# Kernel optimization log

Measured on AMD Instinct MI355X. Metric: run time of the kernel, lower is better.

## Reference

```python
import jax, jax.numpy as jnp
import numpy as np

N_USER = 50000
N_POST = 50000
E = 400000
IN_DIM = 128
HID = 64
HEADS = 4
OUT_DIM = 64
NEG_SLOPE = 0.2


def _xavier(key, shape):
    fan_in, fan_out = shape[0], shape[-1]
    lim = float(np.sqrt(6.0 / (fan_in + fan_out)))
    return jax.random.uniform(key, shape, jnp.float32, -lim, lim)


def setup_inputs() -> dict:
    key = jax.random.key(0)
    ks = jax.random.split(key, 24)
    inp = {}
    inp['x_user'] = jax.random.normal(ks[0], (N_USER, IN_DIM), jnp.float32)
    inp['x_post'] = jax.random.normal(ks[1], (N_POST, IN_DIM), jnp.float32)
    inp['src_u2u'] = jax.random.randint(ks[2], (E,), 0, N_USER, jnp.int32)
    inp['dst_u2u'] = jax.random.randint(ks[3], (E,), 0, N_USER, jnp.int32)
    inp['src_p2u'] = jax.random.randint(ks[4], (E,), 0, N_POST, jnp.int32)
    inp['dst_p2u'] = jax.random.randint(ks[5], (E,), 0, N_USER, jnp.int32)
    inp['src_u2p'] = jax.random.randint(ks[6], (E,), 0, N_USER, jnp.int32)
    inp['dst_u2p'] = jax.random.randint(ks[7], (E,), 0, N_POST, jnp.int32)
    # shared input projection (nn.Linear(in_dim, hidden_dim), xavier W, zero b)
    inp['W_proj'] = _xavier(ks[8], (IN_DIM, HID))
    inp['b_proj'] = jnp.zeros((HID,), jnp.float32)
    # per-edge-type GATConv params: lin [HID, HEADS*HID], att vectors [HEADS, HID], bias [HEADS*HID]
    for i, et in enumerate(['u2u', 'p2u', 'u2p']):
        inp['lin_' + et] = _xavier(ks[9 + 3 * i], (HID, HEADS * HID))
        inp['att_src_' + et] = _xavier(ks[10 + 3 * i], (HEADS, HID))
        inp['att_dst_' + et] = _xavier(ks[11 + 3 * i], (HEADS, HID))
        inp['bias_' + et] = jnp.zeros((HEADS * HID,), jnp.float32)
    inp['W_out'] = _xavier(ks[20], (HEADS * HID, OUT_DIM))
    inp['b_out'] = jnp.zeros((OUT_DIM,), jnp.float32)
    return inp


def _gat_conv(h_src_nodes, h_dst_nodes, src, dst, lin, att_src, att_dst, bias, n_dst):
    # h_*_nodes: [N, HID] projected node features
    hs = (h_src_nodes @ lin).reshape(-1, HEADS, HID)   # [Ns, H, C]
    hd = (h_dst_nodes @ lin).reshape(-1, HEADS, HID)   # [Nd, H, C]
    a_s = jnp.sum(hs * att_src, axis=-1)               # [Ns, H]
    a_d = jnp.sum(hd * att_dst, axis=-1)               # [Nd, H]
    e = jax.nn.leaky_relu(a_s[src] + a_d[dst], NEG_SLOPE)  # [E, H]
    # per-destination segment softmax
    m = jax.lax.stop_gradient(jax.ops.segment_max(e, dst, num_segments=n_dst))
    ex = jnp.exp(e - m[dst])
    s = jax.ops.segment_sum(ex, dst, num_segments=n_dst)
    alpha = ex / (s[dst] + 1e-16)                      # [E, H]
    msg = hs[src] * alpha[:, :, None]                  # [E, H, C]
    out = jax.ops.segment_sum(msg, dst, num_segments=n_dst)  # [Nd, H, C]
    return out.reshape(n_dst, HEADS * HID) + bias


def reference(x_user, x_post, src_u2u, dst_u2u, src_p2u, dst_p2u, src_u2p, dst_u2p,
              W_proj, b_proj,
              lin_u2u, att_src_u2u, att_dst_u2u, bias_u2u,
              lin_p2u, att_src_p2u, att_dst_p2u, bias_p2u,
              lin_u2p, att_src_u2p, att_dst_u2p, bias_u2p,
              W_out, b_out):
    hu = x_user @ W_proj + b_proj   # [N_USER, HID]
    hp = x_post @ W_proj + b_proj   # [N_POST, HID]
    # HeteroConv(aggr='sum'): sum conv outputs sharing the same dst type
    out_user = (_gat_conv(hu, hu, src_u2u, dst_u2u, lin_u2u, att_src_u2u, att_dst_u2u, bias_u2u, N_USER)
                + _gat_conv(hp, hu, src_p2u, dst_p2u, lin_p2u, att_src_p2u, att_dst_p2u, bias_p2u, N_USER))
    out_post = _gat_conv(hu, hp, src_u2p, dst_u2p, lin_u2p, att_src_u2p, att_dst_u2p, bias_u2p, N_POST)
    out_user = jax.nn.elu(out_user)
    out_post = jax.nn.elu(out_post)
    out_user = out_user @ W_out + b_out   # [N_USER, OUT_DIM]
    return (out_user, out_post)
```

## Files before the change

### kernel.cpp

```cpp
#include <hip/hip_runtime.h>
#include <math.h>

#define IN_DIM 128
#define HID 64
#define HEADS 4
#define HH 256
#define OUT_DIM 64
#define NEG_SLOPE 0.2f

typedef unsigned short ushort_t;
using bf16x8 = __attribute__((ext_vector_type(8))) short;
using f32x4  = __attribute__((ext_vector_type(4))) float;

__device__ __forceinline__ float elu_f(float x){ return x > 0.f ? x : (expf(x) - 1.f); }
__device__ __forceinline__ float lrelu_f(float x){ return fmaxf(x, NEG_SLOPE * x); }

__device__ __forceinline__ ushort_t f2bf(float x){
  unsigned u = __float_as_uint(x);
  unsigned r = (u + 0x7fffu + ((u >> 16) & 1u)) >> 16;
  return (ushort_t)r;
}
__device__ __forceinline__ float bf2f(ushort_t v){ return __uint_as_float(((unsigned)v) << 16); }

__global__ void proj_kernel(const float* __restrict__ xu, const float* __restrict__ xp,
                            const float* __restrict__ W, const float* __restrict__ b,
                            float* __restrict__ hu, float* __restrict__ hp,
                            int n_user, int n_total){
  __shared__ float xs[16 * IN_DIM];
  int row0 = blockIdx.x * 16;
  for (int i = threadIdx.x; i < 16 * IN_DIM; i += 256){
    int r = row0 + i / IN_DIM;
    float v = 0.f;
    if (r < n_total){
      int k = i % IN_DIM;
      v = (r < n_user) ? xu[(size_t)r * IN_DIM + k] : xp[(size_t)(r - n_user) * IN_DIM + k];
    }
    xs[i] = v;
  }
  __syncthreads();
  int c = threadIdx.x & 63;
  int g = threadIdx.x >> 6;
  float acc[4] = {0.f, 0.f, 0.f, 0.f};
  for (int k = 0; k < IN_DIM; ++k){
    float wv = W[k * HID + c];
    #pragma unroll
    for (int r = 0; r < 4; ++r) acc[r] += xs[(g * 4 + r) * IN_DIM + k] * wv;
  }
  float bb = b[c];
  #pragma unroll
  for (int r = 0; r < 4; ++r){
    int rr = row0 + g * 4 + r;
    if (rr < n_total){
      float v = acc[r] + bb;
      if (rr < n_user) hu[(size_t)rr * HID + c] = v;
      else             hp[(size_t)(rr - n_user) * HID + c] = v;
    }
  }
}

__global__ void fold3_kernel(const float* __restrict__ lin0, const float* __restrict__ as0, const float* __restrict__ ad0,
                             const float* __restrict__ lin1, const float* __restrict__ as1, const float* __restrict__ ad1,
                             const float* __restrict__ lin2, const float* __restrict__ as2, const float* __restrict__ ad2,
                             float* __restrict__ wbuf){
  int t = blockIdx.x;
  const float* lin = t == 0 ? lin0 : (t == 1 ? lin1 : lin2);
  const float* as  = t == 0 ? as0  : (t == 1 ? as1  : as2);
  const float* ad  = t == 0 ? ad0  : (t == 1 ? ad1  : ad2);
  int tid = threadIdx.x;
  int h = tid >> 6, k = tid & 63;
  float vs = 0.f, vd = 0.f;
  for (int c = 0; c < HID; ++c){
    float lv = lin[k * HH + h * HID + c];
    vs += lv * as[h * HID + c];
    vd += lv * ad[h * HID + c];
  }
  wbuf[(t * 2 + 0) * HH + tid] = vs;
  wbuf[(t * 2 + 1) * HH + tid] = vd;
}

__global__ void att6_kernel(const float* __restrict__ hu, const float* __restrict__ hp,
                            const float* __restrict__ wbuf, float* __restrict__ abuf,
                            int n_user, int n_post, int n_max){
  long gw = ((long)blockIdx.x * blockDim.x + threadIdx.x) >> 6;
  int lane = threadIdx.x & 63;
  int seg, node;
  long r = gw;
  int nu = n_user, np_ = n_post;
  if      (r < nu)            { seg = 0; node = (int)r; }
  else if ((r -= nu) < nu)    { seg = 1; node = (int)r; }
  else if ((r -= nu) < np_)   { seg = 2; node = (int)r; }
  else if ((r -= np_) < nu)   { seg = 3; node = (int)r; }
  else if ((r -= nu) < nu)    { seg = 4; node = (int)r; }
  else if ((r -= nu) < np_)   { seg = 5; node = (int)r; }
  else return;
  const float* h = (seg == 2 || seg == 5) ? hp : hu;
  const float* w = wbuf + seg * HH;
  float* outp = abuf + (size_t)seg * n_max * HEADS;
  float hv = h[(size_t)node * HID + lane];
  #pragma unroll
  for (int hh = 0; hh < HEADS; ++hh){
    float p = hv * w[hh * HID + lane];
    #pragma unroll
    for (int off = 32; off > 0; off >>= 1) p += __shfl_xor(p, off, 64);
    if (lane == 0) outp[(size_t)node * HEADS + hh] = p;
  }
}

__global__ void hist3_kernel(const int* __restrict__ d0, const int* __restrict__ d1,
                             const int* __restrict__ d2, int* __restrict__ deg3,
                             int E0, int E1, int E2, int b1_, int b2_){
  int e = blockIdx.x * blockDim.x + threadIdx.x;
  int ET = E0 + E1 + E2;
  if (e >= ET) return;
  int idx;
  if (e < E0)            idx = d0[e];
  else if (e < E0 + E1)  idx = b1_ + d1[e - E0];
  else                   idx = b2_ + d2[e - E0 - E1];
  atomicAdd(deg3 + idx, 1);
}

__global__ void scan1_kernel(const int* __restrict__ deg, int* __restrict__ offs,
                             int* __restrict__ bsum, int n){
  __shared__ int sm[256];
  int i = blockIdx.x * 256 + threadIdx.x;
  int v = (i < n) ? deg[i] : 0;
  sm[threadIdx.x] = v;
  __syncthreads();
  for (int off = 1; off < 256; off <<= 1){
    int t = (threadIdx.x >= off) ? sm[threadIdx.x - off] : 0;
    __syncthreads();
    sm[threadIdx.x] += t;
    __syncthreads();
  }
  if (i < n) offs[i] = sm[threadIdx.x] - v;
  if (threadIdx.x == 255) bsum[blockIdx.x] = sm[255];
}

__global__ void scan2_kernel(int* __restrict__ bsum, int nb){
  __shared__ int sm[1024];
  int v = (threadIdx.x < nb) ? bsum[threadIdx.x] : 0;
  sm[threadIdx.x] = v;
  __syncthreads();
  for (int off = 1; off < 1024; off <<= 1){
    int t = (threadIdx.x >= off) ? sm[threadIdx.x - off] : 0;
    __syncthreads();
    sm[threadIdx.x] += t;
    __syncthreads();
  }
  if (threadIdx.x < nb) bsum[threadIdx.x] = sm[threadIdx.x] - v;
}

__global__ void scan3_kernel(int* __restrict__ offs, int* __restrict__ cursor,
                             const int* __restrict__ bsum, int n){
  int i = blockIdx.x * 256 + threadIdx.x;
  if (i >= n) return;
  int o = offs[i] + bsum[blockIdx.x];
  offs[i] = o;
  cursor[i] = o;
}

__global__ void csrfill3_kernel(const int* __restrict__ s0, const int* __restrict__ d0,
                                const int* __restrict__ s1, const int* __restrict__ d1,
                                const int* __restrict__ s2, const int* __restrict__ d2,
                                int* __restrict__ cursor, int* __restrict__ csr_src,
                                int E0, int E1, int E2, int b1_, int b2_){
  int e = blockIdx.x * blockDim.x + threadIdx.x;
  int ET = E0 + E1 + E2;
  if (e >= ET) return;
  int sidx, didx;
  if (e < E0){ sidx = s0[e]; didx = d0[e]; }
  else if (e < E0 + E1){ int ee = e - E0; sidx = s1[ee]; didx = b1_ + d1[ee]; }
  else { int ee = e - E0 - E1; sidx = s2[ee]; didx = b2_ + d2[ee]; }
  int pos = atomicAdd(cursor + didx, 1);
  csr_src[pos] = sidx;
}

__global__ void gather_all_kernel(const int* __restrict__ csr_src, const int* __restrict__ offs3,
                                  const int* __restrict__ deg3,
                                  const float* __restrict__ hu, const float* __restrict__ hp,
                                  const float* __restrict__ abuf,
                                  int n_user, int n_post, int n_max,
                                  ushort_t* __restrict__ aggA, ushort_t* __restrict__ aggB,
                                  ushort_t* __restrict__ aggC){
  int gw = blockIdx.x * 4 + (threadIdx.x >> 6);
  int lane = threadIdx.x & 63;
  int n3 = 2 * n_user + n_post;
  if (gw >= n3) return;
  const float* h_src; const float4* as4; const float4* ad4; ushort_t* agg; int dloc;
  size_t astr = (size_t)n_max * HEADS;
  if (gw < n_user){
    dloc = gw; h_src = hu;
    as4 = (const float4*)(abuf + 0 * astr); ad4 = (const float4*)(abuf + 1 * astr); agg = aggA;
  } else if (gw < 2 * n_user){
    dloc = gw - n_user; h_src = hp;
    as4 = (const float4*)(abuf + 2 * astr); ad4 = (const float4*)(abuf + 3 * astr); agg = aggB;
  } else {
    dloc = gw - 2 * n_user; h_src = hu;
    as4 = (const float4*)(abuf + 4 * astr); ad4 = (const float4*)(abuf + 5 * astr); agg = aggC;
  }
  int base = offs3[gw], n = deg3[gw];
  float4 adv = ad4[dloc];
  float s0 = 0.f, s1 = 0.f, s2 = 0.f, s3 = 0.f;
  float a0 = 0.f, a1 = 0.f, a2 = 0.f, a3 = 0.f;
  float hA = 0.f, hB = 0.f;
  float4 aA = make_float4(0,0,0,0), aB = make_float4(0,0,0,0);
  if (n > 0){ int s = csr_src[base];     hA = h_src[(size_t)s * HID + lane]; aA = as4[s]; }
  if (n > 1){ int s = csr_src[base + 1]; hB = h_src[(size_t)s * HID + lane]; aB = as4[s]; }
  for (int j = 0; j < n; ++j){
    float hv = hA; float4 av = aA;
    hA = hB; aA = aB;
    if (j + 2 < n){
      int s = csr_src[base + j + 2];
      hB = h_src[(size_t)s * HID + lane]; aB = as4[s];
    }
    float p0 = __expf(lrelu_f(av.x + adv.x));
    float p1 = __expf(lrelu_f(av.y + adv.y));
    float p2 = __expf(lrelu_f(av.z + adv.z));
    float p3 = __expf(lrelu_f(av.w + adv.w));
    s0 += p0; s1 += p1; s2 += p2; s3 += p3;
    a0 = fmaf(p0, hv, a0); a1 = fmaf(p1, hv, a1);
    a2 = fmaf(p2, hv, a2); a3 = fmaf(p3, hv, a3);
  }
  a0 *= 1.f / (s0 + 1e-16f); a1 *= 1.f / (s1 + 1e-16f);
  a2 *= 1.f / (s2 + 1e-16f); a3 *= 1.f / (s3 + 1e-16f);
  size_t o = (size_t)dloc * HH + lane;
  agg[o + 0 * HID] = f2bf(a0);
  agg[o + 1 * HID] = f2bf(a1);
  agg[o + 2 * HID] = f2bf(a2);
  agg[o + 3 * HID] = f2bf(a3);
}

__global__ void prep_kernel(const float* __restrict__ L0, const float* __restrict__ L1,
                            const float* __restrict__ L2, const float* __restrict__ Wo,
                            const float* __restrict__ b0, const float* __restrict__ b1,
                            ushort_t* __restrict__ Wt0, ushort_t* __restrict__ Wt1,
                            ushort_t* __restrict__ Wt2, ushort_t* __restrict__ Wot,
                            float* __restrict__ bsum){
  int g = blockIdx.x * 256 + threadIdx.x;
  if (g < 49152){
    int m = g >> 14;
    int i = g & 16383;
    int h = i >> 12, rem = i & 4095;
    int o = rem >> 6, c = rem & 63;
    const float* L = m == 0 ? L0 : (m == 1 ? L1 : L2);
    ushort_t* W = m == 0 ? Wt0 : (m == 1 ? Wt1 : Wt2);
    W[i] = f2bf(L[(size_t)c * HH + h * 64 + o]);
  } else if (g < 65536){
    int i = g - 49152;
    int o = i >> 8, k = i & 255;
    Wot[i] = f2bf(Wo[(size_t)k * OUT_DIM + o]);
  } else if (g < 65792){
    int i = g - 65536;
    bsum[i] = b0[i] + b1[i];
  }
}

__global__ void user_epi_mfma(const ushort_t* __restrict__ aggA, const ushort_t* __restrict__ aggB,
                              const ushort_t* __restrict__ Wt0, const ushort_t* __restrict__ Wt1,
                              const ushort_t* __restrict__ Wot, const float* __restrict__ bsum,
                              const float* __restrict__ bo, float* __restrict__ out, int n){
  __shared__ ushort_t Tl[64 * 256];
  int tid = threadIdx.x;
  int w = tid >> 6, lane = tid & 63;
  int l15 = lane & 15, kg = lane >> 4;
  int row0 = blockIdx.x * 64 + w * 16;

  int ar = row0 + l15; if (ar > n - 1) ar = n - 1;
  #pragma unroll
  for (int h = 0; h < HEADS; ++h){
    const ushort_t* pa = aggA + (size_t)ar * HH + h * 64 + kg * 8;
    const ushort_t* pb = aggB + (size_t)ar * HH + h * 64 + kg * 8;
    bf16x8 aA0 = *(const bf16x8*)pa;
    bf16x8 aA1 = *(const bf16x8*)(pa + 32);
    bf16x8 aB0 = *(const bf16x8*)pb;
    bf16x8 aB1 = *(const bf16x8*)(pb + 32);
    #pragma unroll
    for (int n16 = 0; n16 < 4; ++n16){
      int o = n16 * 16 + l15;
      const ushort_t* w0 = Wt0 + h * 4096 + o * 64 + kg * 8;
      const ushort_t* w1 = Wt1 + h * 4096 + o * 64 + kg * 8;
      f32x4 acc = {0.f, 0.f, 0.f, 0.f};
      acc = __builtin_amdgcn_mfma_f32_16x16x32_bf16(aA0, *(const bf16x8*)w0, acc, 0, 0, 0);
      acc = __builtin_amdgcn_mfma_f32_16x16x32_bf16(aA1, *(const bf16x8*)(w0 + 32), acc, 0, 0, 0);
      acc = __builtin_amdgcn_mfma_f32_16x16x32_bf16(aB0, *(const bf16x8*)w1, acc, 0, 0, 0);
      acc = __builtin_amdgcn_mfma_f32_16x16x32_bf16(aB1, *(const bf16x8*)(w1 + 32), acc, 0, 0, 0);
      int col = h * 64 + n16 * 16 + l15;
      float bb = bsum[col];
      #pragma unroll
      for (int j = 0; j < 4; ++j){
        int rl = w * 16 + kg * 4 + j;
        float v = elu_f(acc[j] + bb);
        int byteoff = rl * 512 + ((col * 2) ^ ((rl & 7) << 4));
        Tl[byteoff >> 1] = f2bf(v);
      }
    }
  }
  __syncthreads();

  int rl = w * 16 + l15;
  #pragma unroll
  for (int nf = 0; nf < 4; ++nf){
    f32x4 acc = {0.f, 0.f, 0.f, 0.f};
    const ushort_t* wp = Wot + (nf * 16 + l15) * 256 + kg * 8;
    #pragma unroll
    for (int ks = 0; ks < 8; ++ks){
      int ab = rl * 512 + ((ks * 64 + kg * 16) ^ ((rl & 7) << 4));
      bf16x8 a = *(const bf16x8*)((const char*)Tl + ab);
      acc = __builtin_amdgcn_mfma_f32_16x16x32_bf16(a, *(const bf16x8*)(wp + ks * 32), acc, 0, 0, 0);
    }
    int colo = nf * 16 + l15;
    float bb = bo[colo];
    #pragma unroll
    for (int j = 0; j < 4; ++j){
      int row = blockIdx.x * 64 + w * 16 + kg * 4 + j;
      if (row < n) out[(size_t)row * OUT_DIM + colo] = acc[j] + bb;
    }
  }
}

__global__ void post_epi_mfma(const ushort_t* __restrict__ aggC, const ushort_t* __restrict__ Wt2,
                              const float* __restrict__ b2, float* __restrict__ out, int n){
  int tid = threadIdx.x;
  int w = tid >> 6, lane = tid & 63;
  int l15 = lane & 15, kg = lane >> 4;
  int row0 = blockIdx.x * 64 + w * 16;
  int ar = row0 + l15; if (ar > n - 1) ar = n - 1;
  #pragma unroll
  for (int h = 0; h < HEADS; ++h){
    const ushort_t* pa = aggC + (size_t)ar * HH + h * 64 + kg * 8;
    bf16x8 a0 = *(const bf16x8*)pa;
    bf16x8 a1 = *(const bf16x8*)(pa + 32);
    #pragma unroll
    for (int n16 = 0; n16 < 4; ++n16){
      int o = n16 * 16 + l15;
      const ushort_t* w2 = Wt2 + h * 4096 + o * 64 + kg * 8;
      f32x4 acc = {0.f, 0.f, 0.f, 0.f};
      acc = __builtin_amdgcn_mfma_f32_16x16x32_bf16(a0, *(const bf16x8*)w2, acc, 0, 0, 0);
      acc = __builtin_amdgcn_mfma_f32_16x16x32_bf16(a1, *(const bf16x8*)(w2 + 32), acc, 0, 0, 0);
      int col = h * 64 + n16 * 16 + l15;
      float bb = b2[col];
      #pragma unroll
      for (int j = 0; j < 4; ++j){
        int row = row0 + kg * 4 + j;
        if (row < n) out[(size_t)row * HH + col] = elu_f(acc[j] + bb);
      }
    }
  }
}

extern "C" void kernel_launch(void* const* d_in, const int* in_sizes, int n_in,
                              void* d_out, int out_size, void* d_ws, size_t ws_size,
                              hipStream_t stream){
  const float* xu = (const float*)d_in[0];
  const float* xp = (const float*)d_in[1];
  const float* Wp = (const float*)d_in[8];
  const float* bp = (const float*)d_in[9];
  const float* Wo = (const float*)d_in[22];
  const float* bo = (const float*)d_in[23];

  const int n_user = in_sizes[0] / IN_DIM;
  const int n_post = in_sizes[1] / IN_DIM;
  const int n_max  = n_user > n_post ? n_user : n_post;
  const int E0 = in_sizes[2], E1 = in_sizes[4], E2 = in_sizes[6];
  const int ET = E0 + E1 + E2;
  const int n3 = n_user + n_user + n_post;
  float* out = (float*)d_out;

  float* ws = (float*)d_ws;
  size_t off = 0;
  float* hu       = ws + off; off += (size_t)n_user * HID;
  float* hp       = ws + off; off += (size_t)n_post * HID;
  float* abuf     = ws + off; off += (size_t)6 * n_max * HEADS;
  float* wbuf     = ws + off; off += 6 * HH;
  ushort_t* aggA  = (ushort_t*)(ws + off); off += ((size_t)n_max * HH + 1) / 2;
  ushort_t* aggB  = (ushort_t*)(ws + off); off += ((size_t)n_max * HH + 1) / 2;
  ushort_t* aggC  = (ushort_t*)(ws + off); off += ((size_t)n_max * HH + 1) / 2;
  ushort_t* Wt0   = (ushort_t*)(ws + off); off += 8192;
  ushort_t* Wt1   = (ushort_t*)(ws + off); off += 8192;
  ushort_t* Wt2   = (ushort_t*)(ws + off); off += 8192;
  ushort_t* Wot   = (ushort_t*)(ws + off); off += 8192;
  float* bsum_u   = ws + off; off += 256;
  int* deg3       = (int*)(ws + off); off += n3;
  int* offs3      = (int*)(ws + off); off += n3;
  int* cursor3    = (int*)(ws + off); off += n3;
  int* bsum       = (int*)(ws + off); off += 1024;
  int* csr_src    = (int*)(ws + off); off += ET;

  int n_total = n_user + n_post;
  proj_kernel<<<(n_total + 15) / 16, 256, 0, stream>>>(xu, xp, Wp, bp, hu, hp, n_user, n_total);

  prep_kernel<<<258, 256, 0, stream>>>(
      (const float*)d_in[10], (const float*)d_in[14], (const float*)d_in[18], Wo,
      (const float*)d_in[13], (const float*)d_in[17], Wt0, Wt1, Wt2, Wot, bsum_u);

  fold3_kernel<<<3, 256, 0, stream>>>(
      (const float*)d_in[10], (const float*)d_in[11], (const float*)d_in[12],
      (const float*)d_in[14], (const float*)d_in[15], (const float*)d_in[16],
      (const float*)d_in[18], (const float*)d_in[19], (const float*)d_in[20], wbuf);

  long waves6 = 4L * n_user + 2L * n_post;
  att6_kernel<<<(int)((waves6 + 3) / 4), 256, 0, stream>>>(hu, hp, wbuf, abuf, n_user, n_post, n_max);

  hipMemsetAsync(deg3, 0, (size_t)n3 * sizeof(int), stream);
  hist3_kernel<<<(ET + 255) / 256, 256, 0, stream>>>(
      (const int*)d_in[3], (const int*)d_in[5], (const int*)d_in[7],
      deg3, E0, E1, E2, n_user, 2 * n_user);
  int nb = (n3 + 255) / 256;
  scan1_kernel<<<nb, 256, 0, stream>>>(deg3, offs3, bsum, n3);
  scan2_kernel<<<1, 1024, 0, stream>>>(bsum, nb);
  scan3_kernel<<<nb, 256, 0, stream>>>(offs3, cursor3, bsum, n3);
  csrfill3_kernel<<<(ET + 255) / 256, 256, 0, stream>>>(
      (const int*)d_in[2], (const int*)d_in[3],
      (const int*)d_in[4], (const int*)d_in[5],
      (const int*)d_in[6], (const int*)d_in[7],
      cursor3, csr_src, E0, E1, E2, n_user, 2 * n_user);

  gather_all_kernel<<<(n3 + 3) / 4, 256, 0, stream>>>(
      csr_src, offs3, deg3, hu, hp, abuf, n_user, n_post, n_max, aggA, aggB, aggC);

  user_epi_mfma<<<(n_user + 63) / 64, 256, 0, stream>>>(
      aggA, aggB, Wt0, Wt1, Wot, bsum_u, bo, out, n_user);

  post_epi_mfma<<<(n_post + 63) / 64, 256, 0, stream>>>(
      aggC, Wt2, (const float*)d_in[21], out + (size_t)n_user * OUT_DIM, n_post);
}
```

Before: 632.7 us.

## Use MFMA bf16 input projection, bf16 node features, and precomputed per-edge alpha

Replaces the scalar FP32 input projection with a bf16 MFMA kernel whose weights are transposed in prep. The projected node features are now stored as bf16, which halves the gather traffic. The softmax is split out: a thread-per-node kernel computes normalized per-edge attention weights into a new float4 alpha buffer, and the gather kernel then only does weighted sums. This adds a kernel launch and an extra read and write of 1.2M float4 alphas, and lowers feature precision to bf16.

```diff
diff --git a/kernel.cpp b/kernel.cpp
--- a/kernel.cpp
+++ b/kernel.cpp
@@ -22,38 +22,89 @@
 }
 __device__ __forceinline__ float bf2f(ushort_t v){ return __uint_as_float(((unsigned)v) << 16); }
 
-__global__ void proj_kernel(const float* __restrict__ xu, const float* __restrict__ xp,
-                            const float* __restrict__ W, const float* __restrict__ b,
-                            float* __restrict__ hu, float* __restrict__ hp,
-                            int n_user, int n_total){
-  __shared__ float xs[16 * IN_DIM];
-  int row0 = blockIdx.x * 16;
-  for (int i = threadIdx.x; i < 16 * IN_DIM; i += 256){
-    int r = row0 + i / IN_DIM;
-    float v = 0.f;
-    if (r < n_total){
-      int k = i % IN_DIM;
-      v = (r < n_user) ? xu[(size_t)r * IN_DIM + k] : xp[(size_t)(r - n_user) * IN_DIM + k];
-    }
-    xs[i] = v;
+__global__ void prep_kernel(const float* __restrict__ L0, const float* __restrict__ L1,
+                            const float* __restrict__ L2, const float* __restrict__ Wo,
+                            const float* __restrict__ Wp,
+                            const float* __restrict__ b0, const float* __restrict__ b1,
+                            ushort_t* __restrict__ Wt0, ushort_t* __restrict__ Wt1,
+                            ushort_t* __restrict__ Wt2, ushort_t* __restrict__ Wot,
+                            ushort_t* __restrict__ Wpt, float* __restrict__ bsum){
+  int g = blockIdx.x * 256 + threadIdx.x;
+  if (g < 49152){
+    int m = g >> 14;
+    int i = g & 16383;
+    int h = i >> 12, rem = i & 4095;
+    int o = rem >> 6, c = rem & 63;
+    const float* L = m == 0 ? L0 : (m == 1 ? L1 : L2);
+    ushort_t* W = m == 0 ? Wt0 : (m == 1 ? Wt1 : Wt2);
+    W[i] = f2bf(L[(size_t)c * HH + h * 64 + o]);
+  } else if (g < 65536){
+    int i = g - 49152;
+    int o = i >> 8, k = i & 255;
+    Wot[i] = f2bf(Wo[(size_t)k * OUT_DIM + o]);
+  } else if (g < 73728){
+    int i = g - 65536;
+    int c = i >> 7, k = i & 127;
+    Wpt[i] = f2bf(Wp[(size_t)k * HID + c]);
+  } else if (g < 73984){
+    int i = g - 73728;
+    bsum[i] = b0[i] + b1[i];
+  }
+}
+
+__global__ void proj_mfma(const float* __restrict__ xu, const float* __restrict__ xp,
+                          const ushort_t* __restrict__ Wpt, const float* __restrict__ b,
+                          ushort_t* __restrict__ hu, ushort_t* __restrict__ hp,
+                          int n_user, int n_total){
+  __shared__ ushort_t xs[64 * 128];
+  int tid = threadIdx.x;
+  int row0 = blockIdx.x * 64;
+  #pragma unroll
+  for (int p = 0; p < 4; ++p){
+    int idx = (p * 256 + tid) * 8;
+    int r = idx >> 7, k = idx & 127;
+    int gr = row0 + r;
+    float4 v0 = make_float4(0,0,0,0), v1 = make_float4(0,0,0,0);
+    if (gr < n_total){
+      const float* src = (gr < n_user) ? (xu + (size_t)gr * IN_DIM + k)
+                                       : (xp + (size_t)(gr - n_user) * IN_DIM + k);
+      v0 = *(const float4*)src; v1 = *(const float4*)(src + 4);
+    }
+    bf16x8 bv;
+    bv[0] = (short)f2bf(v0.x); bv[1] = (short)f2bf(v0.y);
+    bv[2] = (short)f2bf(v0.z); bv[3] = (short)f2bf(v0.w);
+    bv[4] = (short)f2bf(v1.x); bv[5] = (short)f2bf(v1.y);
+    bv[6] = (short)f2bf(v1.z); bv[7] = (short)f2bf(v1.w);
+    int byteoff = r * 256 + ((k * 2) ^ ((r & 7) << 4));
+    *(bf16x8*)((char*)xs + byteoff) = bv;
   }
   __syncthreads();
-  int c = threadIdx.x & 63;
-  int g = threadIdx.x >> 6;
-  float acc[4] = {0.f, 0.f, 0.f, 0.f};
-  for (int k = 0; k < IN_DIM; ++k){
-    float wv = W[k * HID + c];
-    #pragma unroll
-    for (int r = 0; r < 4; ++r) acc[r] += xs[(g * 4 + r) * IN_DIM + k] * wv;
-  }
-  float bb = b[c];
-  #pragma unroll
-  for (int r = 0; r < 4; ++r){
-    int rr = row0 + g * 4 + r;
-    if (rr < n_total){
-      float v = acc[r] + bb;
-      if (rr < n_user) hu[(size_t)rr * HID + c] = v;
-      else             hp[(size_t)(rr - n_user) * HID + c] = v;
+  int w = tid >> 6, lane = tid & 63, l15 = lane & 15, kg = lane >> 4;
+  int arow = w * 16 + l15;
+  bf16x8 afrag[4];
+  #pragma unroll
+  for (int ks = 0; ks < 4; ++ks){
+    int k = ks * 32 + kg * 8;
+    int byteoff = arow * 256 + ((k * 2) ^ ((arow & 7) << 4));
+    afrag[ks] = *(const bf16x8*)((const char*)xs + byteoff);
+  }
+  #pragma unroll
+  for (int n16 = 0; n16 < 4; ++n16){
+    f32x4 acc = {0.f, 0.f, 0.f, 0.f};
+    const ushort_t* wp = Wpt + (n16 * 16 + l15) * 128;
+    #pragma unroll
+    for (int ks = 0; ks < 4; ++ks)
+      acc = __builtin_amdgcn_mfma_f32_16x16x32_bf16(afrag[ks], *(const bf16x8*)(wp + ks * 32 + kg * 8), acc, 0, 0, 0);
+    int col = n16 * 16 + l15;
+    float bb = b[col];
+    #pragma unroll
+    for (int j = 0; j < 4; ++j){
+      int row = row0 + w * 16 + kg * 4 + j;
+      if (row < n_total){
+        ushort_t hv = f2bf(acc[j] + bb);
+        if (row < n_user) hu[(size_t)row * HID + col] = hv;
+        else              hp[(size_t)(row - n_user) * HID + col] = hv;
+      }
     }
   }
 }
@@ -78,7 +129,7 @@
   wbuf[(t * 2 + 1) * HH + tid] = vd;
 }
 
-__global__ void att6_kernel(const float* __restrict__ hu, const float* __restrict__ hp,
+__global__ void att6_kernel(const ushort_t* __restrict__ hu, const ushort_t* __restrict__ hp,
                             const float* __restrict__ wbuf, float* __restrict__ abuf,
                             int n_user, int n_post, int n_max){
   long gw = ((long)blockIdx.x * blockDim.x + threadIdx.x) >> 6;
@@ -93,10 +144,10 @@
   else if ((r -= nu) < nu)    { seg = 4; node = (int)r; }
   else if ((r -= nu) < np_)   { seg = 5; node = (int)r; }
   else return;
-  const float* h = (seg == 2 || seg == 5) ? hp : hu;
+  const ushort_t* h = (seg == 2 || seg == 5) ? hp : hu;
   const float* w = wbuf + seg * HH;
   float* outp = abuf + (size_t)seg * n_max * HEADS;
-  float hv = h[(size_t)node * HID + lane];
+  float hv = bf2f(h[(size_t)node * HID + lane]);
   #pragma unroll
   for (int hh = 0; hh < HEADS; ++hh){
     float p = hv * w[hh * HID + lane];
@@ -175,84 +226,72 @@
   csr_src[pos] = sidx;
 }
 
-__global__ void gather_all_kernel(const int* __restrict__ csr_src, const int* __restrict__ offs3,
-                                  const int* __restrict__ deg3,
-                                  const float* __restrict__ hu, const float* __restrict__ hp,
-                                  const float* __restrict__ abuf,
-                                  int n_user, int n_post, int n_max,
-                                  ushort_t* __restrict__ aggA, ushort_t* __restrict__ aggB,
-                                  ushort_t* __restrict__ aggC){
+__global__ void stats_alpha_kernel(const int* __restrict__ csr_src, const int* __restrict__ offs3,
+                                   const int* __restrict__ deg3, const float* __restrict__ abuf,
+                                   float4* __restrict__ alpha,
+                                   int n_user, int n_post, int n_max){
+  int gw = blockIdx.x * 256 + threadIdx.x;
+  int n3 = 2 * n_user + n_post;
+  if (gw >= n3) return;
+  size_t astr = (size_t)n_max;
+  const float4* as4; const float4* ad4; int dloc;
+  const float4* ab = (const float4*)abuf;
+  if (gw < n_user){ dloc = gw; as4 = ab; ad4 = ab + astr; }
+  else if (gw < 2 * n_user){ dloc = gw - n_user; as4 = ab + 2 * astr; ad4 = ab + 3 * astr; }
+  else { dloc = gw - 2 * n_user; as4 = ab + 4 * astr; ad4 = ab + 5 * astr; }
+  int base = offs3[gw], n = deg3[gw];
+  float4 ad = ad4[dloc];
+  float s0 = 0.f, s1 = 0.f, s2 = 0.f, s3 = 0.f;
+  for (int j = 0; j < n; ++j){
+    float4 a = as4[csr_src[base + j]];
+    s0 += __expf(lrelu_f(a.x + ad.x));
+    s1 += __expf(lrelu_f(a.y + ad.y));
+    s2 += __expf(lrelu_f(a.z + ad.z));
+    s3 += __expf(lrelu_f(a.w + ad.w));
+  }
+  float i0 = 1.f / (s0 + 1e-16f), i1 = 1.f / (s1 + 1e-16f);
+  float i2 = 1.f / (s2 + 1e-16f), i3 = 1.f / (s3 + 1e-16f);
+  for (int j = 0; j < n; ++j){
+    float4 a = as4[csr_src[base + j]];
+    alpha[base + j] = make_float4(__expf(lrelu_f(a.x + ad.x)) * i0,
+                                  __expf(lrelu_f(a.y + ad.y)) * i1,
+                                  __expf(lrelu_f(a.z + ad.z)) * i2,
+                                  __expf(lrelu_f(a.w + ad.w)) * i3);
+  }
+}
+
+__global__ void gather_slim(const int* __restrict__ csr_src, const int* __restrict__ offs3,
+                            const int* __restrict__ deg3,
+                            const ushort_t* __restrict__ hu, const ushort_t* __restrict__ hp,
+                            const float4* __restrict__ alpha,
+                            int n_user, int n_post,
+                            ushort_t* __restrict__ aggA, ushort_t* __restrict__ aggB,
+                            ushort_t* __restrict__ aggC){
   int gw = blockIdx.x * 4 + (threadIdx.x >> 6);
   int lane = threadIdx.x & 63;
   int n3 = 2 * n_user + n_post;
   if (gw >= n3) return;
-  const float* h_src; const float4* as4; const float4* ad4; ushort_t* agg; int dloc;
-  size_t astr = (size_t)n_max * HEADS;
-  if (gw < n_user){
-    dloc = gw; h_src = hu;
-    as4 = (const float4*)(abuf + 0 * astr); ad4 = (const float4*)(abuf + 1 * astr); agg = aggA;
-  } else if (gw < 2 * n_user){
-    dloc = gw - n_user; h_src = hp;
-    as4 = (const float4*)(abuf + 2 * astr); ad4 = (const float4*)(abuf + 3 * astr); agg = aggB;
-  } else {
-    dloc = gw - 2 * n_user; h_src = hu;
-    as4 = (const float4*)(abuf + 4 * astr); ad4 = (const float4*)(abuf + 5 * astr); agg = aggC;
-  }
+  const ushort_t* h; ushort_t* agg; int dloc;
+  if (gw < n_user){ dloc = gw; h = hu; agg = aggA; }
+  else if (gw < 2 * n_user){ dloc = gw - n_user; h = hp; agg = aggB; }
+  else { dloc = gw - 2 * n_user; h = hu; agg = aggC; }
   int base = offs3[gw], n = deg3[gw];
-  float4 adv = ad4[dloc];
-  float s0 = 0.f, s1 = 0.f, s2 = 0.f, s3 = 0.f;
   float a0 = 0.f, a1 = 0.f, a2 = 0.f, a3 = 0.f;
   float hA = 0.f, hB = 0.f;
-  float4 aA = make_float4(0,0,0,0), aB = make_float4(0,0,0,0);
-  if (n > 0){ int s = csr_src[base];     hA = h_src[(size_t)s * HID + lane]; aA = as4[s]; }
-  if (n > 1){ int s = csr_src[base + 1]; hB = h_src[(size_t)s * HID + lane]; aB = as4[s]; }
+  if (n > 0) hA = bf2f(h[(size_t)csr_src[base] * HID + lane]);
+  if (n > 1) hB = bf2f(h[(size_t)csr_src[base + 1] * HID + lane]);
   for (int j = 0; j < n; ++j){
-    float hv = hA; float4 av = aA;
-    hA = hB; aA = aB;
-    if (j + 2 < n){
-      int s = csr_src[base + j + 2];
-      hB = h_src[(size_t)s * HID + lane]; aB = as4[s];
-    }
-    float p0 = __expf(lrelu_f(av.x + adv.x));
-    float p1 = __expf(lrelu_f(av.y + adv.y));
-    float p2 = __expf(lrelu_f(av.z + adv.z));
-    float p3 = __expf(lrelu_f(av.w + adv.w));
-    s0 += p0; s1 += p1; s2 += p2; s3 += p3;
-    a0 = fmaf(p0, hv, a0); a1 = fmaf(p1, hv, a1);
-    a2 = fmaf(p2, hv, a2); a3 = fmaf(p3, hv, a3);
-  }
-  a0 *= 1.f / (s0 + 1e-16f); a1 *= 1.f / (s1 + 1e-16f);
-  a2 *= 1.f / (s2 + 1e-16f); a3 *= 1.f / (s3 + 1e-16f);
+    float hv = hA; hA = hB;
+    if (j + 2 < n) hB = bf2f(h[(size_t)csr_src[base + j + 2] * HID + lane]);
+    float4 al = alpha[base + j];
+    a0 = fmaf(al.x, hv, a0); a1 = fmaf(al.y, hv, a1);
+    a2 = fmaf(al.z, hv, a2); a3 = fmaf(al.w, hv, a3);
+  }
   size_t o = (size_t)dloc * HH + lane;
   agg[o + 0 * HID] = f2bf(a0);
   agg[o + 1 * HID] = f2bf(a1);
   agg[o + 2 * HID] = f2bf(a2);
   agg[o + 3 * HID] = f2bf(a3);
-}
-
-__global__ void prep_kernel(const float* __restrict__ L0, const float* __restrict__ L1,
-                            const float* __restrict__ L2, const float* __restrict__ Wo,
-                            const float* __restrict__ b0, const float* __restrict__ b1,
-                            ushort_t* __restrict__ Wt0, ushort_t* __restrict__ Wt1,
-                            ushort_t* __restrict__ Wt2, ushort_t* __restrict__ Wot,
-                            float* __restrict__ bsum){
-  int g = blockIdx.x * 256 + threadIdx.x;
-  if (g < 49152){
-    int m = g >> 14;
-    int i = g & 16383;
-    int h = i >> 12, rem = i & 4095;
-    int o = rem >> 6, c = rem & 63;
-    const float* L = m == 0 ? L0 : (m == 1 ? L1 : L2);
-    ushort_t* W = m == 0 ? Wt0 : (m == 1 ? Wt1 : Wt2);
-    W[i] = f2bf(L[(size_t)c * HH + h * 64 + o]);
-  } else if (g < 65536){
-    int i = g - 49152;
-    int o = i >> 8, k = i & 255;
-    Wot[i] = f2bf(Wo[(size_t)k * OUT_DIM + o]);
-  } else if (g < 65792){
-    int i = g - 65536;
-    bsum[i] = b0[i] + b1[i];
-  }
 }
 
 __global__ void user_epi_mfma(const ushort_t* __restrict__ aggA, const ushort_t* __restrict__ aggB,
@@ -368,30 +407,34 @@
 
   float* ws = (float*)d_ws;
   size_t off = 0;
-  float* hu       = ws + off; off += (size_t)n_user * HID;
-  float* hp       = ws + off; off += (size_t)n_post * HID;
+  ushort_t* hu    = (ushort_t*)(ws + off); off += (size_t)n_user * HID / 2;
+  ushort_t* hp    = (ushort_t*)(ws + off); off += (size_t)n_post * HID / 2;
   float* abuf     = ws + off; off += (size_t)6 * n_max * HEADS;
   float* wbuf     = ws + off; off += 6 * HH;
-  ushort_t* aggA  = (ushort_t*)(ws + off); off += ((size_t)n_max * HH + 1) / 2;
-  ushort_t* aggB  = (ushort_t*)(ws + off); off += ((size_t)n_max * HH + 1) / 2;
-  ushort_t* aggC  = (ushort_t*)(ws + off); off += ((size_t)n_max * HH + 1) / 2;
+  ushort_t* aggA  = (ushort_t*)(ws + off); off += (size_t)n_max * HH / 2;
+  ushort_t* aggB  = (ushort_t*)(ws + off); off += (size_t)n_max * HH / 2;
+  ushort_t* aggC  = (ushort_t*)(ws + off); off += (size_t)n_max * HH / 2;
   ushort_t* Wt0   = (ushort_t*)(ws + off); off += 8192;
   ushort_t* Wt1   = (ushort_t*)(ws + off); off += 8192;
   ushort_t* Wt2   = (ushort_t*)(ws + off); off += 8192;
   ushort_t* Wot   = (ushort_t*)(ws + off); off += 8192;
+  ushort_t* Wpt   = (ushort_t*)(ws + off); off += 4096;
   float* bsum_u   = ws + off; off += 256;
   int* deg3       = (int*)(ws + off); off += n3;
   int* offs3      = (int*)(ws + off); off += n3;
   int* cursor3    = (int*)(ws + off); off += n3;
   int* bsum       = (int*)(ws + off); off += 1024;
   int* csr_src    = (int*)(ws + off); off += ET;
+  off = (off + 3) & ~(size_t)3;
+  float4* alpha   = (float4*)(ws + off); off += (size_t)ET * 4;
 
   int n_total = n_user + n_post;
-  proj_kernel<<<(n_total + 15) / 16, 256, 0, stream>>>(xu, xp, Wp, bp, hu, hp, n_user, n_total);
-
-  prep_kernel<<<258, 256, 0, stream>>>(
-      (const float*)d_in[10], (const float*)d_in[14], (const float*)d_in[18], Wo,
-      (const float*)d_in[13], (const float*)d_in[17], Wt0, Wt1, Wt2, Wot, bsum_u);
+
+  prep_kernel<<<289, 256, 0, stream>>>(
+      (const float*)d_in[10], (const float*)d_in[14], (const float*)d_in[18], Wo, Wp,
+      (const float*)d_in[13], (const float*)d_in[17], Wt0, Wt1, Wt2, Wot, Wpt, bsum_u);
+
+  proj_mfma<<<(n_total + 63) / 64, 256, 0, stream>>>(xu, xp, Wpt, bp, hu, hp, n_user, n_total);
 
   fold3_kernel<<<3, 256, 0, stream>>>(
       (const float*)d_in[10], (const float*)d_in[11], (const float*)d_in[12],
@@ -415,8 +458,11 @@
       (const int*)d_in[6], (const int*)d_in[7],
       cursor3, csr_src, E0, E1, E2, n_user, 2 * n_user);
 
-  gather_all_kernel<<<(n3 + 3) / 4, 256, 0, stream>>>(
-      csr_src, offs3, deg3, hu, hp, abuf, n_user, n_post, n_max, aggA, aggB, aggC);
+  stats_alpha_kernel<<<(n3 + 255) / 256, 256, 0, stream>>>(
+      csr_src, offs3, deg3, abuf, alpha, n_user, n_post, n_max);
+
+  gather_slim<<<(n3 + 3) / 4, 256, 0, stream>>>(
+      csr_src, offs3, deg3, hu, hp, alpha, n_user, n_post, aggA, aggB, aggC);
 
   user_epi_mfma<<<(n_user + 63) / 64, 256, 0, stream>>>(
       aggA, aggB, Wt0, Wt1, Wot, bsum_u, bo, out, n_user);
```

Result: slower. 688.6 us (+8.8%).
